# Performance work log

Hardware: AMD Instinct MI355X
Metric: run time of the kernel (lower is better)

The kernel has to match this reference:

```python
import jax, jax.numpy as jnp
import numpy as np

NP, NO, E, IN_DIM, D = 100000, 200000, 500000, 512, 256
EPS = 1e-12  # torch F.normalize default eps


def setup_inputs() -> dict:
    key = jax.random.key(0)
    ks = jax.random.split(key, 12)
    return {
        "feat_prefix": jax.random.normal(ks[0], (NP, IN_DIM), jnp.float32),
        "feat_other": jax.random.normal(ks[1], (NO, IN_DIM), jnp.float32),
        "src": jax.random.randint(ks[2], (E,), 0, NP),
        "dst": jax.random.randint(ks[3], (E,), 0, NO),
        "Wm_p": jax.random.normal(ks[4], (IN_DIM, D), jnp.float32) * 0.02,
        "bm_p": jax.random.normal(ks[5], (D,), jnp.float32) * 0.02,
        "Wm_o": jax.random.normal(ks[6], (IN_DIM, D), jnp.float32) * 0.02,
        "bm_o": jax.random.normal(ks[7], (D,), jnp.float32) * 0.02,
        "W": jax.random.normal(ks[8], (D, D), jnp.float32) * 0.02,
        "bW": jax.random.normal(ks[9], (D,), jnp.float32) * 0.02,
        "a_w": jax.random.normal(ks[10], (2 * D,), jnp.float32) * 0.02,
        "a_b": jax.random.normal(ks[11], (1,), jnp.float32) * 0.02,
    }


def _l2norm(x):
    n = jnp.linalg.norm(x, axis=-1, keepdims=True)
    return x / jnp.maximum(n, EPS)


def reference(feat_prefix, feat_other, src, dst,
              Wm_p, bm_p, Wm_o, bm_o, W, bW, a_w, a_b):
    # FeatureMappingLayer: per-ntype Linear + ReLU
    hp = jax.nn.relu(feat_prefix @ Wm_p + bm_p)   # [NP, D]
    ho = jax.nn.relu(feat_other @ Wm_o + bm_o)    # [NO, D]
    d = hp.shape[1]
    n_prefix = hp.shape[0]

    # GAT-style score: a([W h_src ; W h_dst]) -- project at node level,
    # decompose the concat-linear into two per-node dot products, then gather.
    hp_proj = hp @ W + bW                         # [NP, D]
    ho_proj = ho @ W + bW                         # [NO, D]
    s_src = hp_proj @ a_w[:d]                     # [NP]
    s_dst = ho_proj @ a_w[d:]                     # [NO]
    e = s_src[src] + s_dst[dst] + a_b[0]          # [E] per-edge scores

    # Segment softmax over source (Prefix) node
    m = jax.ops.segment_max(e, src, num_segments=n_prefix)
    m = jnp.where(jnp.isfinite(m), m, 0.0)        # empty segments -> 0
    ex = jnp.exp(e - m[src])
    denom = jax.ops.segment_sum(ex, src, num_segments=n_prefix)
    alpha = ex / denom[src]                       # [E]

    # Scatter-weighted sum of mapped (pre-W) dst features into Prefix nodes
    agg = jax.ops.segment_sum(alpha[:, None] * ho[dst], src,
                              num_segments=n_prefix)  # [NP, D]

    return (_l2norm(agg), _l2norm(ho))
```

## Files before the change

### kernel.cpp

```cpp
#include <hip/hip_runtime.h>
#include <math.h>

#define IN_DIM 512
#define DD 256

typedef _Float16 half8_t __attribute__((ext_vector_type(8)));
typedef _Float16 half4_t __attribute__((ext_vector_type(4)));
typedef __attribute__((ext_vector_type(4))) float f32x4_t;

__global__ void prep_w2(const float* __restrict__ W, const float* __restrict__ a_w,
                        float* __restrict__ w2) {
  int i = threadIdx.x;
  float s = 0.f;
  for (int j = 0; j < DD; ++j) s = fmaf(W[i * DD + j], a_w[DD + j], s);
  w2[i] = s;
}

__global__ void bconv_kernel(const float* __restrict__ Wm, _Float16* __restrict__ Bh) {
  int i = blockIdx.x * 256 + threadIdx.x;
  int k = i >> 8, col = i & 255;
  int kc16 = k >> 5, kr = k & 31;
  int lane = ((kr >> 3) << 4) | (col & 15);
  int nf = col >> 4;
  int off = (((((kc16 << 4) + nf) << 6) + lane) << 3) + (kr & 7);
  Bh[off] = (_Float16)Wm[i];
}

__device__ __forceinline__ half8_t cvt8(const float4& a, const float4& b) {
  half8_t h;
  h[0] = (_Float16)a.x; h[1] = (_Float16)a.y; h[2] = (_Float16)a.z; h[3] = (_Float16)a.w;
  h[4] = (_Float16)b.x; h[5] = (_Float16)b.y; h[6] = (_Float16)b.z; h[7] = (_Float16)b.w;
  return h;
}

__global__ __launch_bounds__(256, 3) void map_gemm_mfma(
    const float* __restrict__ X, const _Float16* __restrict__ Bh,
    const float* __restrict__ bm, const float* __restrict__ w2,
    float* __restrict__ Yn, _Float16* __restrict__ Y16,
    float* __restrict__ wnorm, int M) {
  __shared__ ushort Ah[2][8192];
  const int t = threadIdx.x;
  const int w = t >> 6;
  const int l = t & 63;
  const int c = l & 15;
  const int g = l >> 4;
  const int row0 = blockIdx.x * 64;

  const int sr = t >> 2;
  const int skb = (t & 3) << 5;
  int gr = row0 + sr;
  if (gr >= M) gr = M - 1;
  const float* xrow = X + (size_t)gr * IN_DIM;

  f32x4_t acc[4][4];
#pragma unroll
  for (int m = 0; m < 4; ++m)
#pragma unroll
    for (int n = 0; n < 4; ++n) acc[m][n] = (f32x4_t){0.f, 0.f, 0.f, 0.f};

  const int sw = (sr & 15) << 3;
  const int i0 = (sr << 7) + skb;
  const half8_t* bhb = reinterpret_cast<const half8_t*>(Bh);

  float4 r0, r1, r2, r3, r4, r5, r6, r7;
  {
    const float4* p = reinterpret_cast<const float4*>(xrow + skb);
    r0 = p[0]; r1 = p[1]; r2 = p[2]; r3 = p[3];
    r4 = p[4]; r5 = p[5]; r6 = p[6]; r7 = p[7];
    *reinterpret_cast<half8_t*>(&Ah[0][(i0 + 0) ^ sw]) = cvt8(r0, r1);
    *reinterpret_cast<half8_t*>(&Ah[0][(i0 + 8) ^ sw]) = cvt8(r2, r3);
    *reinterpret_cast<half8_t*>(&Ah[0][(i0 + 16) ^ sw]) = cvt8(r4, r5);
    *reinterpret_cast<half8_t*>(&Ah[0][(i0 + 24) ^ sw]) = cvt8(r6, r7);
  }
  __syncthreads();

  for (int ks = 0; ks < 4; ++ks) {
    const int cur = ks & 1;
    if (ks < 3) {
      const float4* p = reinterpret_cast<const float4*>(xrow + ((ks + 1) << 7) + skb);
      r0 = p[0]; r1 = p[1]; r2 = p[2]; r3 = p[3];
      r4 = p[4]; r5 = p[5]; r6 = p[6]; r7 = p[7];
    }

#pragma unroll
    for (int kc = 0; kc < 4; ++kc) {
      const int kc16 = (ks << 2) + kc;
      half8_t ah[4];
#pragma unroll
      for (int m = 0; m < 4; ++m) {
        int r = (m << 4) + c;
        int idx = ((r << 7) + (kc << 5) + (g << 3)) ^ (c << 3);
        ah[m] = *reinterpret_cast<const half8_t*>(&Ah[cur][idx]);
      }
      half8_t bh[4];
#pragma unroll
      for (int n = 0; n < 4; ++n)
        bh[n] = bhb[(((kc16 << 4) + (w << 2) + n) << 6) + l];
#pragma unroll
      for (int n = 0; n < 4; ++n)
#pragma unroll
        for (int m = 0; m < 4; ++m)
          acc[m][n] = __builtin_amdgcn_mfma_f32_16x16x32_f16(ah[m], bh[n], acc[m][n], 0, 0, 0);
    }

    if (ks < 3) {
      const int nxt = cur ^ 1;
      *reinterpret_cast<half8_t*>(&Ah[nxt][(i0 + 0) ^ sw]) = cvt8(r0, r1);
      *reinterpret_cast<half8_t*>(&Ah[nxt][(i0 + 8) ^ sw]) = cvt8(r2, r3);
      *reinterpret_cast<half8_t*>(&Ah[nxt][(i0 + 16) ^ sw]) = cvt8(r4, r5);
      *reinterpret_cast<half8_t*>(&Ah[nxt][(i0 + 24) ^ sw]) = cvt8(r6, r7);
    }
    __syncthreads();
  }

  float bv[4], wv[4];
#pragma unroll
  for (int n = 0; n < 4; ++n) {
    bv[n] = bm[(w << 6) + (n << 4) + c];
    wv[n] = w2[(w << 6) + (n << 4) + c];
  }
#pragma unroll
  for (int m = 0; m < 4; ++m)
#pragma unroll
    for (int n = 0; n < 4; ++n)
#pragma unroll
      for (int q = 0; q < 4; ++q) {
        float v = acc[m][n][q] + bv[n];
        acc[m][n][q] = v > 0.f ? v : 0.f;
      }

  float* red = reinterpret_cast<float*>(&Ah[0][0]);
  float pss[4][4], pdt[4][4];
#pragma unroll
  for (int m = 0; m < 4; ++m)
#pragma unroll
    for (int q = 0; q < 4; ++q) {
      float ss = 0.f, dt = 0.f;
#pragma unroll
      for (int n = 0; n < 4; ++n) {
        float a = acc[m][n][q];
        ss = fmaf(a, a, ss);
        dt = fmaf(a, wv[n], dt);
      }
      for (int d = 8; d; d >>= 1) {
        ss += __shfl_down(ss, d, 16);
        dt += __shfl_down(dt, d, 16);
      }
      pss[m][q] = ss;
      pdt[m][q] = dt;
    }
  __syncthreads();
#pragma unroll
  for (int m = 0; m < 4; ++m)
#pragma unroll
    for (int q = 0; q < 4; ++q)
      if (c == 0) {
        int rr = (m << 4) + (g << 2) + q;
        red[(w << 6) + rr] = pss[m][q];
        red[256 + (w << 6) + rr] = pdt[m][q];
      }
  __syncthreads();
  if (t < 64) {
    float ss = red[t] + red[64 + t] + red[128 + t] + red[192 + t];
    float dt = red[256 + t] + red[320 + t] + red[384 + t] + red[448 + t];
    float nr = sqrtf(ss);
    red[512 + t] = 1.f / fmaxf(nr, 1e-12f);
    int r = row0 + t;
    if (r < M) wnorm[r] = expf(dt) * nr;
  }
  __syncthreads();
#pragma unroll
  for (int m = 0; m < 4; ++m)
#pragma unroll
    for (int q = 0; q < 4; ++q) {
      int rr = (m << 4) + (g << 2) + q;
      float sc = red[512 + rr];
      int r = row0 + rr;
      if (r < M) {
#pragma unroll
        for (int n = 0; n < 4; ++n) {
          float v = acc[m][n][q] * sc;
          int col = (w << 6) + (n << 4) + c;
          Yn[(size_t)r * DD + col] = v;
          Y16[(size_t)r * DD + col] = (_Float16)v;
        }
      }
    }
}

__global__ void hist_kernel(const int* __restrict__ src, int* __restrict__ deg, int E) {
  int i = blockIdx.x * blockDim.x + threadIdx.x;
  if (i < E) atomicAdd(&deg[src[i]], 1);
}

__global__ __launch_bounds__(256) void scan_part(const int* __restrict__ deg,
                                                 int* __restrict__ bsum, int NP) {
  __shared__ int s[256];
  int t = threadIdx.x, b = blockIdx.x;
  int i0 = (b * 256 + t) * 2;
  int v0 = (i0 < NP) ? deg[i0] : 0;
  int v1 = (i0 + 1 < NP) ? deg[i0 + 1] : 0;
  s[t] = v0 + v1;
  __syncthreads();
  for (int off = 128; off; off >>= 1) {
    if (t < off) s[t] += s[t + off];
    __syncthreads();
  }
  if (t == 0) bsum[b] = s[0];
}

__global__ __launch_bounds__(256) void scan_top(int* __restrict__ bsum,
                                                int* __restrict__ rowptr_last) {
  __shared__ int s[256];
  int t = threadIdx.x;
  int v = bsum[t];
  s[t] = v;
  __syncthreads();
  for (int off = 1; off < 256; off <<= 1) {
    int u = (t >= off) ? s[t - off] : 0;
    __syncthreads();
    s[t] += u;
    __syncthreads();
  }
  bsum[t] = s[t] - v;
  if (t == 255) *rowptr_last = s[255];
}

__global__ __launch_bounds__(256) void scan_fin(const int* __restrict__ deg,
                                                const int* __restrict__ bsum,
                                                int* __restrict__ rowptr,
                                                int* __restrict__ cursor, int NP) {
  __shared__ int s[256];
  int t = threadIdx.x, b = blockIdx.x;
  int i0 = (b * 256 + t) * 2;
  int v0 = (i0 < NP) ? deg[i0] : 0;
  int v1 = (i0 + 1 < NP) ? deg[i0 + 1] : 0;
  int local = v0 + v1;
  s[t] = local;
  __syncthreads();
  for (int off = 1; off < 256; off <<= 1) {
    int u = (t >= off) ? s[t - off] : 0;
    __syncthreads();
    s[t] += u;
    __syncthreads();
  }
  int base = bsum[b] + s[t] - local;
  if (i0 < NP) { rowptr[i0] = base; cursor[i0] = base; }
  if (i0 + 1 < NP) { rowptr[i0 + 1] = base + v0; cursor[i0 + 1] = base + v0; }
}

__global__ void fill_kernel(const int* __restrict__ src, const int* __restrict__ dst,
                            int* __restrict__ cursor, int* __restrict__ ebuf, int E) {
  int i = blockIdx.x * blockDim.x + threadIdx.x;
  if (i < E) {
    int pos = atomicAdd(&cursor[src[i]], 1);
    ebuf[pos] = dst[i];
  }
}

__global__ void agg_kernel(const int* __restrict__ rowptr, const int* __restrict__ ebuf,
                           const float* __restrict__ wnorm, const _Float16* __restrict__ hon16,
                           float* __restrict__ agg, int NP) {
  int p = (int)(((long)blockIdx.x * blockDim.x + threadIdx.x) >> 6);
  int lane = threadIdx.x & 63;
  if (p >= NP) return;
  int beg = rowptr[p], end = rowptr[p + 1];
  float4 acc = {0.f, 0.f, 0.f, 0.f};
  if (beg < end) {
    int d0 = ebuf[beg];
    float w0 = wnorm[d0];
    half4_t v0 = *reinterpret_cast<const half4_t*>(&hon16[(size_t)d0 * DD + lane * 4]);
    float w1 = 0.f;
    half4_t v1 = {0, 0, 0, 0};
    if (beg + 1 < end) {
      int d1 = ebuf[beg + 1];
      w1 = wnorm[d1];
      v1 = *reinterpret_cast<const half4_t*>(&hon16[(size_t)d1 * DD + lane * 4]);
    }
    for (int j = beg; j < end; ++j) {
      float wn_ = 0.f;
      half4_t vn = {0, 0, 0, 0};
      if (j + 2 < end) {
        int dn = ebuf[j + 2];
        wn_ = wnorm[dn];
        vn = *reinterpret_cast<const half4_t*>(&hon16[(size_t)dn * DD + lane * 4]);
      }
      acc.x = fmaf(w0, (float)v0[0], acc.x);
      acc.y = fmaf(w0, (float)v0[1], acc.y);
      acc.z = fmaf(w0, (float)v0[2], acc.z);
      acc.w = fmaf(w0, (float)v0[3], acc.w);
      w0 = w1; v0 = v1; w1 = wn_; v1 = vn;
    }
  }
  float ss = acc.x * acc.x + acc.y * acc.y + acc.z * acc.z + acc.w * acc.w;
#pragma unroll
  for (int d = 32; d > 0; d >>= 1) ss += __shfl_xor(ss, d, 64);
  float inv = 1.0f / fmaxf(sqrtf(ss), 1e-12f);
  float4 o = {acc.x * inv, acc.y * inv, acc.z * inv, acc.w * inv};
  *reinterpret_cast<float4*>(&agg[(size_t)p * DD + lane * 4]) = o;
}

extern "C" void kernel_launch(void* const* d_in, const int* in_sizes, int n_in,
                              void* d_out, int out_size, void* d_ws, size_t ws_size,
                              hipStream_t stream) {
  const float* feat_other = (const float*)d_in[1];
  const int* src = (const int*)d_in[2];
  const int* dst = (const int*)d_in[3];
  const float* Wm_o = (const float*)d_in[6];
  const float* bm_o = (const float*)d_in[7];
  const float* W = (const float*)d_in[8];
  const float* a_w = (const float*)d_in[10];

  const int NP = in_sizes[0] / IN_DIM;
  const int NO = in_sizes[1] / IN_DIM;
  const int E = in_sizes[2];

  float* out = (float*)d_out;
  float* agg_out = out;
  float* ho_out = out + (size_t)NP * DD;

  float* ws = (float*)d_ws;
  float* wnorm = ws;
  float* w2 = wnorm + NO;
  int* deg = (int*)(w2 + 256);
  int* rowptr = deg + NP;
  int* cursor = rowptr + NP + 1;
  int* bsum = cursor + NP;
  int* ebuf = bsum + 256;
  size_t foff = (size_t)NO + 256 + NP + (NP + 1) + NP + 256 + E;
  foff = (foff + 3) & ~(size_t)3;
  _Float16* Bh = (_Float16*)(ws + foff);
  _Float16* Y16 = Bh + (size_t)IN_DIM * DD;

  hipMemsetAsync(deg, 0, (size_t)NP * sizeof(int), stream);

  prep_w2<<<1, 256, 0, stream>>>(W, a_w, w2);
  bconv_kernel<<<(IN_DIM * DD) / 256, 256, 0, stream>>>(Wm_o, Bh);

  map_gemm_mfma<<<(NO + 63) / 64, 256, 0, stream>>>(
      feat_other, Bh, bm_o, w2, ho_out, Y16, wnorm, NO);

  hist_kernel<<<(E + 255) / 256, 256, 0, stream>>>(src, deg, E);
  scan_part<<<256, 256, 0, stream>>>(deg, bsum, NP);
  scan_top<<<1, 256, 0, stream>>>(bsum, rowptr + NP);
  scan_fin<<<256, 256, 0, stream>>>(deg, bsum, rowptr, cursor, NP);
  fill_kernel<<<(E + 255) / 256, 256, 0, stream>>>(src, dst, cursor, ebuf, E);

  agg_kernel<<<(NP * 64 + 255) / 256, 256, 0, stream>>>(
      rowptr, ebuf, wnorm, Y16, agg_out, NP);
}
```

Measured before the change: 388.8 us.

## Deepen GEMM global prefetch to two stages and parallelize w2 prep

The mapping GEMM now keeps two k-slices of the input rows in registers, so global loads are issued two steps ahead instead of one. Launch bounds are relaxed from three to two blocks per SM to make room for the extra registers. prep_w2 is rewritten to use one wavefront per row, with vector loads and a shuffle reduction across 64 blocks, replacing a single serial block. The deeper prefetch hides more memory latency but costs registers and possibly occupancy.

```diff
diff --git a/kernel.cpp b/kernel.cpp
--- a/kernel.cpp
+++ b/kernel.cpp
@@ -8,12 +8,18 @@
 typedef _Float16 half4_t __attribute__((ext_vector_type(4)));
 typedef __attribute__((ext_vector_type(4))) float f32x4_t;
 
-__global__ void prep_w2(const float* __restrict__ W, const float* __restrict__ a_w,
-                        float* __restrict__ w2) {
-  int i = threadIdx.x;
-  float s = 0.f;
-  for (int j = 0; j < DD; ++j) s = fmaf(W[i * DD + j], a_w[DD + j], s);
-  w2[i] = s;
+__global__ __launch_bounds__(256) void prep_w2(const float* __restrict__ W,
+                                               const float* __restrict__ a_w,
+                                               float* __restrict__ w2) {
+  int row = (blockIdx.x * 256 + threadIdx.x) >> 6;
+  int lane = threadIdx.x & 63;
+  if (row >= DD) return;
+  float4 wv = *reinterpret_cast<const float4*>(&W[(size_t)row * DD + lane * 4]);
+  float4 av = *reinterpret_cast<const float4*>(&a_w[DD + lane * 4]);
+  float s = wv.x * av.x + wv.y * av.y + wv.z * av.z + wv.w * av.w;
+#pragma unroll
+  for (int d = 32; d; d >>= 1) s += __shfl_xor(s, d, 64);
+  if (lane == 0) w2[row] = s;
 }
 
 __global__ void bconv_kernel(const float* __restrict__ Wm, _Float16* __restrict__ Bh) {
@@ -33,7 +39,7 @@
   return h;
 }
 
-__global__ __launch_bounds__(256, 3) void map_gemm_mfma(
+__global__ __launch_bounds__(256, 2) void map_gemm_mfma(
     const float* __restrict__ X, const _Float16* __restrict__ Bh,
     const float* __restrict__ bm, const float* __restrict__ w2,
     float* __restrict__ Yn, _Float16* __restrict__ Y16,
@@ -62,24 +68,28 @@
   const int i0 = (sr << 7) + skb;
   const half8_t* bhb = reinterpret_cast<const half8_t*>(Bh);
 
-  float4 r0, r1, r2, r3, r4, r5, r6, r7;
+  float4 st[2][8];
   {
-    const float4* p = reinterpret_cast<const float4*>(xrow + skb);
-    r0 = p[0]; r1 = p[1]; r2 = p[2]; r3 = p[3];
-    r4 = p[4]; r5 = p[5]; r6 = p[6]; r7 = p[7];
-    *reinterpret_cast<half8_t*>(&Ah[0][(i0 + 0) ^ sw]) = cvt8(r0, r1);
-    *reinterpret_cast<half8_t*>(&Ah[0][(i0 + 8) ^ sw]) = cvt8(r2, r3);
-    *reinterpret_cast<half8_t*>(&Ah[0][(i0 + 16) ^ sw]) = cvt8(r4, r5);
-    *reinterpret_cast<half8_t*>(&Ah[0][(i0 + 24) ^ sw]) = cvt8(r6, r7);
-  }
-  __syncthreads();
-
+    const float4* p0 = reinterpret_cast<const float4*>(xrow + skb);
+    const float4* p1 = reinterpret_cast<const float4*>(xrow + 128 + skb);
+#pragma unroll
+    for (int i = 0; i < 8; ++i) st[0][i] = p0[i];
+#pragma unroll
+    for (int i = 0; i < 8; ++i) st[1][i] = p1[i];
+    *reinterpret_cast<half8_t*>(&Ah[0][(i0 + 0) ^ sw]) = cvt8(st[0][0], st[0][1]);
+    *reinterpret_cast<half8_t*>(&Ah[0][(i0 + 8) ^ sw]) = cvt8(st[0][2], st[0][3]);
+    *reinterpret_cast<half8_t*>(&Ah[0][(i0 + 16) ^ sw]) = cvt8(st[0][4], st[0][5]);
+    *reinterpret_cast<half8_t*>(&Ah[0][(i0 + 24) ^ sw]) = cvt8(st[0][6], st[0][7]);
+  }
+  __syncthreads();
+
+#pragma unroll
   for (int ks = 0; ks < 4; ++ks) {
     const int cur = ks & 1;
-    if (ks < 3) {
-      const float4* p = reinterpret_cast<const float4*>(xrow + ((ks + 1) << 7) + skb);
-      r0 = p[0]; r1 = p[1]; r2 = p[2]; r3 = p[3];
-      r4 = p[4]; r5 = p[5]; r6 = p[6]; r7 = p[7];
+    if (ks < 2) {
+      const float4* p = reinterpret_cast<const float4*>(xrow + ((ks + 2) << 7) + skb);
+#pragma unroll
+      for (int i = 0; i < 8; ++i) st[ks & 1][i] = p[i];
     }
 
 #pragma unroll
@@ -105,10 +115,11 @@
 
     if (ks < 3) {
       const int nxt = cur ^ 1;
-      *reinterpret_cast<half8_t*>(&Ah[nxt][(i0 + 0) ^ sw]) = cvt8(r0, r1);
-      *reinterpret_cast<half8_t*>(&Ah[nxt][(i0 + 8) ^ sw]) = cvt8(r2, r3);
-      *reinterpret_cast<half8_t*>(&Ah[nxt][(i0 + 16) ^ sw]) = cvt8(r4, r5);
-      *reinterpret_cast<half8_t*>(&Ah[nxt][(i0 + 24) ^ sw]) = cvt8(r6, r7);
+      const int sidx = (ks + 1) & 1;
+      *reinterpret_cast<half8_t*>(&Ah[nxt][(i0 + 0) ^ sw]) = cvt8(st[sidx][0], st[sidx][1]);
+      *reinterpret_cast<half8_t*>(&Ah[nxt][(i0 + 8) ^ sw]) = cvt8(st[sidx][2], st[sidx][3]);
+      *reinterpret_cast<half8_t*>(&Ah[nxt][(i0 + 16) ^ sw]) = cvt8(st[sidx][4], st[sidx][5]);
+      *reinterpret_cast<half8_t*>(&Ah[nxt][(i0 + 24) ^ sw]) = cvt8(st[sidx][6], st[sidx][7]);
     }
     __syncthreads();
   }
@@ -334,7 +345,7 @@
 
   hipMemsetAsync(deg, 0, (size_t)NP * sizeof(int), stream);
 
-  prep_w2<<<1, 256, 0, stream>>>(W, a_w, w2);
+  prep_w2<<<64, 256, 0, stream>>>(W, a_w, w2);
   bconv_kernel<<<(IN_DIM * DD) / 256, 256, 0, stream>>>(Wm_o, Bh);
 
   map_gemm_mfma<<<(NO + 63) / 64, 256, 0, stream>>>(
```

Result: faster. 376.2 us (-3.2%).
